# Kernel tuning notes

Measured on AMD Instinct MI355X. Metric: run time of the kernel, lower is better.

## Reference

```python
import jax, jax.numpy as jnp
import numpy as np
import math

B, N, KN, CIN, COUT, NC, DIM = 4, 8192, 16, 64, 64, 16, 3


def _linear_params(key, fan_in, fan_out):
    kw, kb = jax.random.split(key)
    bound = 1.0 / math.sqrt(fan_in)
    w = jax.random.uniform(kw, (fan_in, fan_out), jnp.float32, -bound, bound)
    b = jax.random.uniform(kb, (fan_out,), jnp.float32, -bound, bound)
    return w, b


def setup_inputs() -> dict:
    key = jax.random.key(0)
    ks = jax.random.split(key, 9)
    inp = jax.random.normal(ks[0], (B, N, CIN), jnp.float32)
    points = jax.random.uniform(ks[1], (B, N, DIM), jnp.float32)
    next_pts = jax.random.uniform(ks[2], (B, N, DIM), jnp.float32)
    indices = jax.random.randint(ks[3], (B, N, KN), 0, N, jnp.int64)
    wbound = math.sqrt(3.0) * math.sqrt(2.0 / (CIN + COUT))
    weight = jax.random.uniform(ks[4], (CIN, NC, COUT), jnp.float32, -wbound, wbound)
    bias = jnp.zeros((COUT,), jnp.float32)
    # centers: points inside the unit ball (scaled uniform cube is a faithful stand-in for a learned param init)
    centers = jax.random.uniform(ks[5], (DIM, NC), jnp.float32, -1.0, 1.0) / math.sqrt(DIM)
    l1_w, l1_b = _linear_params(ks[6], DIM * NC, 2 * NC)
    l2_w, l2_b = _linear_params(ks[7], 2 * NC, NC)
    l3_w, l3_b = _linear_params(ks[8], NC, NC)
    return {
        "inp": inp, "points": points, "next_pts": next_pts, "indices": indices,
        "weight": weight, "bias": bias, "centers": centers,
        "l1_w": l1_w, "l1_b": l1_b, "l2_w": l2_w, "l2_b": l2_b,
        "l3_w": l3_w, "l3_b": l3_b, "K": KN,
    }


def reference(inp, points, next_pts, indices, weight, bias, centers,
              l1_w, l1_b, l2_w, l2_b, l3_w, l3_b, K):
    b, n, cin = inp.shape
    bidx = jnp.arange(b)[:, None, None]
    feats = inp[bidx, indices]                                # [B, N, K, Cin] gather
    pts = points[bidx, indices] - next_pts[:, :, None, :]     # [B, N, K, D] relative coords
    # distances to kernel centers -> flatten to [B, N, K, D*NC]
    d = (pts[..., :, None] - centers).reshape(b, n, K, -1)
    d = jax.nn.relu(d @ l1_w + l1_b)
    d = jax.nn.relu(d @ l2_w + l2_b)
    d = jax.nn.relu(d @ l3_w + l3_b)                          # [B, N, K, NC]
    f = jnp.einsum('bnkc,bnkm->bncm', feats, d).reshape(b, n, -1)  # [B, N, Cin*NC]
    out = (f @ weight.reshape(-1, weight.shape[-1])) / K + bias    # [B, N, Cout]
    return out
```

## Files before the change

### kernel.cpp

```cpp
#include <hip/hip_runtime.h>

#define BB    4
#define NN    8192
#define KK    16
#define CIN   64
#define COUTC 64
#define P     16

typedef short bf16x8 __attribute__((ext_vector_type(8)));
typedef float f32x4  __attribute__((ext_vector_type(4)));
typedef float f32x2  __attribute__((ext_vector_type(2)));
typedef unsigned short u16x4 __attribute__((ext_vector_type(4)));

__device__ __forceinline__ unsigned short f2bf_rne(float f) {
    unsigned int u = __builtin_bit_cast(unsigned int, f);
    u += 0x7fffu + ((u >> 16) & 1u);
    return (unsigned short)(u >> 16);
}

__device__ __forceinline__ unsigned int pack_bf2(float lo, float hi) {
    return (unsigned int)f2bf_rne(lo) | ((unsigned int)f2bf_rne(hi) << 16);
}

__global__ __launch_bounds__(256) void prep_all(
    const float* __restrict__ inp, unsigned short* __restrict__ inp_bf,
    const float* __restrict__ W, unsigned short* __restrict__ Wt,
    const float* __restrict__ l1w, const float* __restrict__ l1b,
    const float* __restrict__ centers, float* __restrict__ A1)
{
    const int blk = blockIdx.x;
    const int t   = threadIdx.x;
    if (blk < 8192) {
        const int o  = blk * 256 + t;
        const int n  = o >> 6;
        const int q  = o & 63;
        const int r  = q >> 2;
        const int t4 = q & 3;
        inp_bf[o] = f2bf_rne(inp[n * 64 + t4 * 16 + r]);
    } else if (blk < 8448) {
        const int o    = (blk - 8192) * 256 + t;
        const int cout = o >> 10;
        const int kp   = o & 1023;
        const int m    = kp >> 6;
        const int cin  = kp & 63;
        Wt[o] = f2bf_rne(W[(cin * 16 + m) * 64 + cout] * (1.0f / 16.0f));
    } else if (t < 32) {
        float bb = l1b[t];
        float a0 = 0.f, a1 = 0.f, a2 = 0.f;
        for (int c = 0; c < 16; ++c) {
            const float w0 = l1w[(c     ) * 32 + t];
            const float w1 = l1w[(16 + c) * 32 + t];
            const float w2 = l1w[(32 + c) * 32 + t];
            a0 += w0; a1 += w1; a2 += w2;
            bb -= centers[c] * w0 + centers[16 + c] * w1 + centers[32 + c] * w2;
        }
        A1[0 * 32 + t] = a0; A1[1 * 32 + t] = a1; A1[2 * 32 + t] = a2; A1[3 * 32 + t] = bb;
    }
}

__global__ __launch_bounds__(256, 2) void ptconv_fused(
    const unsigned short* __restrict__ inp_bf,
    const float* __restrict__ points,
    const float* __restrict__ next_pts,
    const int*   __restrict__ indices,
    const unsigned short* __restrict__ Wt,
    const float* __restrict__ A1f,
    const float* __restrict__ bias,
    const float* __restrict__ l2w, const float* __restrict__ l2b,
    const float* __restrict__ l3w, const float* __restrict__ l3b,
    float* __restrict__ out)
{
    const int t    = threadIdx.x;
    const int lane = t & 63;
    const int w    = t >> 6;
    const int pt0  = blockIdx.x * P;
    const int b    = pt0 >> 13;

    __shared__ unsigned short s_u[P][512];

    const f32x2 zero2 = {0.f, 0.f};

    {
        const int p = t >> 4, k = t & 15;
        const int pt = pt0 + p;
        const int id = indices[(size_t)pt0 * KK + t];
        const float* pp = points + ((size_t)(b * NN + id)) * 3;
        const float* np = next_pts + (size_t)pt * 3;
        const float px = pp[0] - np[0];
        const float py = pp[1] - np[1];
        const float pz = pp[2] - np[2];
        const f32x2 px2 = {px, px}, py2 = {py, py}, pz2 = {pz, pz};

        const f32x2* A0  = (const f32x2*)(A1f);
        const f32x2* A1v = (const f32x2*)(A1f + 32);
        const f32x2* A2  = (const f32x2*)(A1f + 64);
        const f32x2* A3  = (const f32x2*)(A1f + 96);
        f32x2 h1[16];
        #pragma unroll
        for (int j = 0; j < 16; ++j) {
            f32x2 a = __builtin_elementwise_fma(pz2, A2[j], A3[j]);
            a = __builtin_elementwise_fma(py2, A1v[j], a);
            a = __builtin_elementwise_fma(px2, A0[j], a);
            h1[j] = __builtin_elementwise_max(a, zero2);
        }

        f32x2 h2[8];
        {
            const f32x2* b2p = (const f32x2*)l2b;
            #pragma unroll
            for (int j = 0; j < 8; ++j) h2[j] = b2p[j];
        }
        #pragma unroll
        for (int i = 0; i < 32; ++i) {
            const float hv = h1[i >> 1][i & 1];
            const f32x2 hvv = {hv, hv};
            const f32x2* wr = (const f32x2*)(l2w + i * 16);
            #pragma unroll
            for (int j = 0; j < 8; ++j)
                h2[j] = __builtin_elementwise_fma(hvv, wr[j], h2[j]);
        }
        #pragma unroll
        for (int j = 0; j < 8; ++j) h2[j] = __builtin_elementwise_max(h2[j], zero2);

        f32x2 h3v[8];
        {
            const f32x2* b3p = (const f32x2*)l3b;
            #pragma unroll
            for (int j = 0; j < 8; ++j) h3v[j] = b3p[j];
        }
        #pragma unroll
        for (int i = 0; i < 16; ++i) {
            const float hv = h2[i >> 1][i & 1];
            const f32x2 hvv = {hv, hv};
            const f32x2* wr = (const f32x2*)(l3w + i * 16);
            #pragma unroll
            for (int j = 0; j < 8; ++j)
                h3v[j] = __builtin_elementwise_fma(hvv, wr[j], h3v[j]);
        }
        char* ub = (char*)s_u;
        const unsigned int hsw = ((unsigned)(p & 3)) << 5;
        #pragma unroll
        for (int j = 0; j < 8; ++j) {
            const f32x2 v = __builtin_elementwise_max(h3v[j], zero2);
            const unsigned int b0 = ((unsigned)(p * 1024 + (2 * j    ) * 32 + k * 2)) ^ hsw;
            const unsigned int b1 = ((unsigned)(p * 1024 + (2 * j + 1) * 32 + k * 2)) ^ hsw;
            *(unsigned short*)(ub + b0) = f2bf_rne(v[0]);
            *(unsigned short*)(ub + b1) = f2bf_rne(v[1]);
        }
    }
    __threadfence_block();

    uint2 holdA[2][2], holdB[2][2];
    {
        const int arow = lane & 15;
        const int hi   = lane >> 4;
        const int kg   = (hi & 1) * 8;
        const unsigned short* ibase = inp_bf + (size_t)b * NN * 64;
        const int* idxg = indices + (size_t)pt0 * KK;
        const bf16x8 vzero = {0, 0, 0, 0, 0, 0, 0, 0};
        char* fbb = (char*)s_u;

        #pragma unroll
        for (int pr = 0; pr < 2; ++pr) {
            const int pA  = w * 4 + pr * 2;
            const int pB  = pA + 1;
            const int myp = (hi < 2) ? pA : pB;

            const int4 i0 = *(const int4*)&idxg[myp * 16 + kg];
            const int4 i1 = *(const int4*)&idxg[myp * 16 + kg + 4];
            const int ids[8] = {i0.x, i0.y, i0.z, i0.w, i1.x, i1.y, i1.z, i1.w};

            u16x4 rows[8];
            #pragma unroll
            for (int jj = 0; jj < 8; ++jj)
                rows[jj] = *(const u16x4*)(ibase + (size_t)ids[jj] * 64 + arow * 4);

            const unsigned int hb = ((unsigned)(myp * 1024 + arow * 32 + kg * 2))
                                    ^ (((unsigned)(myp & 3)) << 5);
            const bf16x8 vfull = *(const bf16x8*)((const char*)s_u + hb);
            const bf16x8 bfA = (hi < 2) ? vfull : vzero;
            const bf16x8 bfB = (hi < 2) ? vzero : vfull;

            #pragma unroll
            for (int tile = 0; tile < 4; ++tile) {
                bf16x8 af;
                #pragma unroll
                for (int jj = 0; jj < 8; ++jj) af[jj] = (short)rows[jj][tile];
                const f32x4 z4 = {0.f, 0.f, 0.f, 0.f};
                const f32x4 dA = __builtin_amdgcn_mfma_f32_16x16x32_bf16(af, bfA, z4, 0, 0, 0);
                const f32x4 dB = __builtin_amdgcn_mfma_f32_16x16x32_bf16(af, bfB, z4, 0, 0, 0);
                const uint2 vA = make_uint2(pack_bf2(dA[0], dA[1]), pack_bf2(dA[2], dA[3]));
                const uint2 vB = make_uint2(pack_bf2(dB[0], dB[1]), pack_bf2(dB[2], dB[3]));
                if (tile < 2) {
                    const unsigned int baseo = (unsigned)(arow * 64 + tile * 32 + hi * 8);
                    const unsigned int offA = ((unsigned)(pA * 1024) + baseo)
                                              ^ (((unsigned)((pA & 7) ^ (arow & 7))) << 4);
                    const unsigned int offB = ((unsigned)(pB * 1024) + baseo)
                                              ^ (((unsigned)((pB & 7) ^ (arow & 7))) << 4);
                    *(uint2*)(fbb + offA) = vA;
                    *(uint2*)(fbb + offB) = vB;
                } else {
                    holdA[pr][tile - 2] = vA;
                    holdB[pr][tile - 2] = vB;
                }
            }
        }
    }
    __syncthreads();

    {
        const int arow = lane & 15;
        const int hi   = lane >> 4;
        const unsigned short* wb = Wt + (size_t)(w * 16 + arow) * 1024 + hi * 8;
        const char* fbb = (const char*)s_u;
        f32x4 acc = {0.f, 0.f, 0.f, 0.f};

        #pragma unroll
        for (int m = 0; m < 16; ++m) {
            const unsigned int xr = ((unsigned)((arow & 7) ^ (m & 7))) << 4;
            const bf16x8 av = *(const bf16x8*)(fbb +
                (((unsigned)(arow * 1024 + m * 64 + hi * 16)) ^ xr));
            const bf16x8 bv = *(const bf16x8*)(wb + m * 64);
            acc = __builtin_amdgcn_mfma_f32_16x16x32_bf16(av, bv, acc, 0, 0, 0);
        }
        __syncthreads();

        {
            char* fbw = (char*)s_u;
            #pragma unroll
            for (int pr = 0; pr < 2; ++pr) {
                const int pA = w * 4 + pr * 2;
                const int pB = pA + 1;
                #pragma unroll
                for (int t2 = 0; t2 < 2; ++t2) {
                    const unsigned int baseo = (unsigned)(arow * 64 + t2 * 32 + hi * 8);
                    const unsigned int offA = ((unsigned)(pA * 1024) + baseo)
                                              ^ (((unsigned)((pA & 7) ^ (arow & 7))) << 4);
                    const unsigned int offB = ((unsigned)(pB * 1024) + baseo)
                                              ^ (((unsigned)((pB & 7) ^ (arow & 7))) << 4);
                    *(uint2*)(fbw + offA) = holdA[pr][t2];
                    *(uint2*)(fbw + offB) = holdB[pr][t2];
                }
            }
        }
        __syncthreads();

        #pragma unroll
        for (int m = 0; m < 16; ++m) {
            const unsigned int xr = ((unsigned)((arow & 7) ^ (m & 7))) << 4;
            const bf16x8 av = *(const bf16x8*)(fbb +
                (((unsigned)(arow * 1024 + m * 64 + hi * 16)) ^ xr));
            const bf16x8 bv = *(const bf16x8*)(wb + m * 64 + 32);
            acc = __builtin_amdgcn_mfma_f32_16x16x32_bf16(av, bv, acc, 0, 0, 0);
        }

        const float bvs = bias[w * 16 + arow];
        #pragma unroll
        for (int r = 0; r < 4; ++r) {
            const int prow = hi * 4 + r;
            out[((size_t)(pt0 + prow)) * 64 + w * 16 + arow] = acc[r] + bvs;
        }
    }
}

extern "C" void kernel_launch(void* const* d_in, const int* in_sizes, int n_in,
                              void* d_out, int out_size, void* d_ws, size_t ws_size,
                              hipStream_t stream) {
    const float* inp      = (const float*)d_in[0];
    const float* points   = (const float*)d_in[1];
    const float* next_pts = (const float*)d_in[2];
    const int*   indices  = (const int*)  d_in[3];
    const float* weight   = (const float*)d_in[4];
    const float* bias     = (const float*)d_in[5];
    const float* centers  = (const float*)d_in[6];
    const float* l1w      = (const float*)d_in[7];
    const float* l1b      = (const float*)d_in[8];
    const float* l2w      = (const float*)d_in[9];
    const float* l2b      = (const float*)d_in[10];
    const float* l3w      = (const float*)d_in[11];
    const float* l3b      = (const float*)d_in[12];
    float* outp = (float*)d_out;

    unsigned short* Wt    = (unsigned short*)d_ws;
    float*          A1f   = (float*)((char*)d_ws + 131072);
    unsigned short* inpbf = (unsigned short*)((char*)d_ws + (1 << 20));

    prep_all<<<8449, 256, 0, stream>>>(inp, inpbf, weight, Wt,
                                       l1w, l1b, centers, A1f);

    const int grid = (BB * NN) / P;
    ptconv_fused<<<grid, 256, 0, stream>>>(inpbf, points, next_pts, indices,
                                           Wt, A1f, bias,
                                           l2w, l2b, l3w, l3b, outp);
}
```

Measured before the change: 57.03 us.

## Process 32 points per block, reusing weight fragments across two MFMA tiles

Doubles the points handled per block from 16 to 32. Each thread now runs the per-neighbour MLP for two neighbours, each wave gathers and transposes twice as many point pairs, and the final GEMM issues two MFMAs per loaded weight fragment. This halves the global weight reads per point and the per-block overhead. In exchange it doubles shared memory and the held registers per block and halves the grid size, which may reduce occupancy.

Result: faster. 54.51 us (-4.4%).

```diff
diff --git a/kernel.cpp b/kernel.cpp
--- a/kernel.cpp
+++ b/kernel.cpp
@@ -5,7 +5,7 @@
 #define KK    16
 #define CIN   64
 #define COUTC 64
-#define P     16
+#define P     32
 
 typedef short bf16x8 __attribute__((ext_vector_type(8)));
 typedef float f32x4  __attribute__((ext_vector_type(4)));
@@ -81,76 +81,84 @@
     const f32x2 zero2 = {0.f, 0.f};
 
     {
-        const int p = t >> 4, k = t & 15;
+        const int p  = w * 8 + (lane >> 3);
+        const int kb = lane & 7;
         const int pt = pt0 + p;
-        const int id = indices[(size_t)pt0 * KK + t];
-        const float* pp = points + ((size_t)(b * NN + id)) * 3;
         const float* np = next_pts + (size_t)pt * 3;
-        const float px = pp[0] - np[0];
-        const float py = pp[1] - np[1];
-        const float pz = pp[2] - np[2];
-        const f32x2 px2 = {px, px}, py2 = {py, py}, pz2 = {pz, pz};
+        const float nx = np[0], ny = np[1], nz = np[2];
 
         const f32x2* A0  = (const f32x2*)(A1f);
         const f32x2* A1v = (const f32x2*)(A1f + 32);
         const f32x2* A2  = (const f32x2*)(A1f + 64);
         const f32x2* A3  = (const f32x2*)(A1f + 96);
-        f32x2 h1[16];
-        #pragma unroll
-        for (int j = 0; j < 16; ++j) {
-            f32x2 a = __builtin_elementwise_fma(pz2, A2[j], A3[j]);
-            a = __builtin_elementwise_fma(py2, A1v[j], a);
-            a = __builtin_elementwise_fma(px2, A0[j], a);
-            h1[j] = __builtin_elementwise_max(a, zero2);
-        }
-
-        f32x2 h2[8];
-        {
-            const f32x2* b2p = (const f32x2*)l2b;
-            #pragma unroll
-            for (int j = 0; j < 8; ++j) h2[j] = b2p[j];
-        }
-        #pragma unroll
-        for (int i = 0; i < 32; ++i) {
-            const float hv = h1[i >> 1][i & 1];
-            const f32x2 hvv = {hv, hv};
-            const f32x2* wr = (const f32x2*)(l2w + i * 16);
-            #pragma unroll
-            for (int j = 0; j < 8; ++j)
-                h2[j] = __builtin_elementwise_fma(hvv, wr[j], h2[j]);
-        }
-        #pragma unroll
-        for (int j = 0; j < 8; ++j) h2[j] = __builtin_elementwise_max(h2[j], zero2);
-
-        f32x2 h3v[8];
-        {
-            const f32x2* b3p = (const f32x2*)l3b;
-            #pragma unroll
-            for (int j = 0; j < 8; ++j) h3v[j] = b3p[j];
-        }
-        #pragma unroll
-        for (int i = 0; i < 16; ++i) {
-            const float hv = h2[i >> 1][i & 1];
-            const f32x2 hvv = {hv, hv};
-            const f32x2* wr = (const f32x2*)(l3w + i * 16);
-            #pragma unroll
-            for (int j = 0; j < 8; ++j)
-                h3v[j] = __builtin_elementwise_fma(hvv, wr[j], h3v[j]);
-        }
-        char* ub = (char*)s_u;
-        const unsigned int hsw = ((unsigned)(p & 3)) << 5;
-        #pragma unroll
-        for (int j = 0; j < 8; ++j) {
-            const f32x2 v = __builtin_elementwise_max(h3v[j], zero2);
-            const unsigned int b0 = ((unsigned)(p * 1024 + (2 * j    ) * 32 + k * 2)) ^ hsw;
-            const unsigned int b1 = ((unsigned)(p * 1024 + (2 * j + 1) * 32 + k * 2)) ^ hsw;
-            *(unsigned short*)(ub + b0) = f2bf_rne(v[0]);
-            *(unsigned short*)(ub + b1) = f2bf_rne(v[1]);
+
+        #pragma unroll
+        for (int ii = 0; ii < 2; ++ii) {
+            const int k  = kb + ii * 8;
+            const int id = indices[(size_t)pt0 * KK + p * 16 + k];
+            const float* pp = points + ((size_t)(b * NN + id)) * 3;
+            const float px = pp[0] - nx;
+            const float py = pp[1] - ny;
+            const float pz = pp[2] - nz;
+            const f32x2 px2 = {px, px}, py2 = {py, py}, pz2 = {pz, pz};
+
+            f32x2 h1[16];
+            #pragma unroll
+            for (int j = 0; j < 16; ++j) {
+                f32x2 a = __builtin_elementwise_fma(pz2, A2[j], A3[j]);
+                a = __builtin_elementwise_fma(py2, A1v[j], a);
+                a = __builtin_elementwise_fma(px2, A0[j], a);
+                h1[j] = __builtin_elementwise_max(a, zero2);
+            }
+
+            f32x2 h2[8];
+            {
+                const f32x2* b2p = (const f32x2*)l2b;
+                #pragma unroll
+                for (int j = 0; j < 8; ++j) h2[j] = b2p[j];
+            }
+            #pragma unroll
+            for (int i = 0; i < 32; ++i) {
+                const float hv = h1[i >> 1][i & 1];
+                const f32x2 hvv = {hv, hv};
+                const f32x2* wr = (const f32x2*)(l2w + i * 16);
+                #pragma unroll
+                for (int j = 0; j < 8; ++j)
+                    h2[j] = __builtin_elementwise_fma(hvv, wr[j], h2[j]);
+            }
+            #pragma unroll
+            for (int j = 0; j < 8; ++j) h2[j] = __builtin_elementwise_max(h2[j], zero2);
+
+            f32x2 h3v[8];
+            {
+                const f32x2* b3p = (const f32x2*)l3b;
+                #pragma unroll
+                for (int j = 0; j < 8; ++j) h3v[j] = b3p[j];
+            }
+            #pragma unroll
+            for (int i = 0; i < 16; ++i) {
+                const float hv = h2[i >> 1][i & 1];
+                const f32x2 hvv = {hv, hv};
+                const f32x2* wr = (const f32x2*)(l3w + i * 16);
+                #pragma unroll
+                for (int j = 0; j < 8; ++j)
+                    h3v[j] = __builtin_elementwise_fma(hvv, wr[j], h3v[j]);
+            }
+            char* ub = (char*)s_u;
+            const unsigned int hsw = ((unsigned)(p & 3)) << 5;
+            #pragma unroll
+            for (int j = 0; j < 8; ++j) {
+                const f32x2 v = __builtin_elementwise_max(h3v[j], zero2);
+                const unsigned int b0 = ((unsigned)(p * 1024 + (2 * j    ) * 32 + k * 2)) ^ hsw;
+                const unsigned int b1 = ((unsigned)(p * 1024 + (2 * j + 1) * 32 + k * 2)) ^ hsw;
+                *(unsigned short*)(ub + b0) = f2bf_rne(v[0]);
+                *(unsigned short*)(ub + b1) = f2bf_rne(v[1]);
+            }
         }
     }
     __threadfence_block();
 
-    uint2 holdA[2][2], holdB[2][2];
+    uint2 holdA[4][2], holdB[4][2];
     {
         const int arow = lane & 15;
         const int hi   = lane >> 4;
@@ -161,8 +169,8 @@
         char* fbb = (char*)s_u;
 
         #pragma unroll
-        for (int pr = 0; pr < 2; ++pr) {
-            const int pA  = w * 4 + pr * 2;
+        for (int pr = 0; pr < 4; ++pr) {
+            const int pA  = w * 8 + pr * 2;
             const int pB  = pA + 1;
             const int myp = (hi < 2) ? pA : pB;
 
@@ -213,23 +221,27 @@
         const int hi   = lane >> 4;
         const unsigned short* wb = Wt + (size_t)(w * 16 + arow) * 1024 + hi * 8;
         const char* fbb = (const char*)s_u;
-        f32x4 acc = {0.f, 0.f, 0.f, 0.f};
+        f32x4 acc0 = {0.f, 0.f, 0.f, 0.f};
+        f32x4 acc1 = {0.f, 0.f, 0.f, 0.f};
 
         #pragma unroll
         for (int m = 0; m < 16; ++m) {
             const unsigned int xr = ((unsigned)((arow & 7) ^ (m & 7))) << 4;
-            const bf16x8 av = *(const bf16x8*)(fbb +
+            const bf16x8 bv  = *(const bf16x8*)(wb + m * 64);
+            const bf16x8 av0 = *(const bf16x8*)(fbb +
                 (((unsigned)(arow * 1024 + m * 64 + hi * 16)) ^ xr));
-            const bf16x8 bv = *(const bf16x8*)(wb + m * 64);
-            acc = __builtin_amdgcn_mfma_f32_16x16x32_bf16(av, bv, acc, 0, 0, 0);
+            const bf16x8 av1 = *(const bf16x8*)(fbb +
+                (((unsigned)((16 + arow) * 1024 + m * 64 + hi * 16)) ^ xr));
+            acc0 = __builtin_amdgcn_mfma_f32_16x16x32_bf16(av0, bv, acc0, 0, 0, 0);
+            acc1 = __builtin_amdgcn_mfma_f32_16x16x32_bf16(av1, bv, acc1, 0, 0, 0);
         }
         __syncthreads();
 
         {
             char* fbw = (char*)s_u;
             #pragma unroll
-            for (int pr = 0; pr < 2; ++pr) {
-                const int pA = w * 4 + pr * 2;
+            for (int pr = 0; pr < 4; ++pr) {
+                const int pA = w * 8 + pr * 2;
                 const int pB = pA + 1;
                 #pragma unroll
                 for (int t2 = 0; t2 < 2; ++t2) {
@@ -248,17 +260,21 @@
         #pragma unroll
         for (int m = 0; m < 16; ++m) {
             const unsigned int xr = ((unsigned)((arow & 7) ^ (m & 7))) << 4;
-            const bf16x8 av = *(const bf16x8*)(fbb +
+            const bf16x8 bv  = *(const bf16x8*)(wb + m * 64 + 32);
+            const bf16x8 av0 = *(const bf16x8*)(fbb +
                 (((unsigned)(arow * 1024 + m * 64 + hi * 16)) ^ xr));
-            const bf16x8 bv = *(const bf16x8*)(wb + m * 64 + 32);
-            acc = __builtin_amdgcn_mfma_f32_16x16x32_bf16(av, bv, acc, 0, 0, 0);
+            const bf16x8 av1 = *(const bf16x8*)(fbb +
+                (((unsigned)((16 + arow) * 1024 + m * 64 + hi * 16)) ^ xr));
+            acc0 = __builtin_amdgcn_mfma_f32_16x16x32_bf16(av0, bv, acc0, 0, 0, 0);
+            acc1 = __builtin_amdgcn_mfma_f32_16x16x32_bf16(av1, bv, acc1, 0, 0, 0);
         }
 
         const float bvs = bias[w * 16 + arow];
         #pragma unroll
         for (int r = 0; r < 4; ++r) {
             const int prow = hi * 4 + r;
-            out[((size_t)(pt0 + prow)) * 64 + w * 16 + arow] = acc[r] + bvs;
+            out[((size_t)(pt0 + prow)) * 64 + w * 16 + arow]      = acc0[r] + bvs;
+            out[((size_t)(pt0 + 16 + prow)) * 64 + w * 16 + arow] = acc1[r] + bvs;
         }
     }
 }
```

## Run the per-neighbor MLP layers 2 and 3 on bf16 MFMA via LDS staging

Applied to the files above, without the earlier changes.

The second and third layers of the per-neighbor weight MLP were scalar fp32 FMA loops per thread (about 768 FMAs each). They now run as bf16 16x16x32 MFMAs. Layer-1 activations are packed to bf16 and staged in a per-wave LDS region, and pre-transposed bf16 copies of l2w/l3w (zero-padded for layer 3) are built in the prep kernel. This removes a large scalar ALU and register cost in exchange for extra LDS round trips, wave-local fences, and bf16 rounding of the intermediate activations.

After: 53.13 us. 1.07x faster.

```diff
diff --git a/kernel.cpp b/kernel.cpp
--- a/kernel.cpp
+++ b/kernel.cpp
@@ -26,7 +26,9 @@
     const float* __restrict__ inp, unsigned short* __restrict__ inp_bf,
     const float* __restrict__ W, unsigned short* __restrict__ Wt,
     const float* __restrict__ l1w, const float* __restrict__ l1b,
-    const float* __restrict__ centers, float* __restrict__ A1)
+    const float* __restrict__ centers, float* __restrict__ A1,
+    const float* __restrict__ l2w, const float* __restrict__ l3w,
+    unsigned short* __restrict__ Wt2, unsigned short* __restrict__ Wt3)
 {
     const int blk = blockIdx.x;
     const int t   = threadIdx.x;
@@ -44,17 +46,32 @@
         const int m    = kp >> 6;
         const int cin  = kp & 63;
         Wt[o] = f2bf_rne(W[(cin * 16 + m) * 64 + cout] * (1.0f / 16.0f));
-    } else if (t < 32) {
-        float bb = l1b[t];
-        float a0 = 0.f, a1 = 0.f, a2 = 0.f;
-        for (int c = 0; c < 16; ++c) {
-            const float w0 = l1w[(c     ) * 32 + t];
-            const float w1 = l1w[(16 + c) * 32 + t];
-            const float w2 = l1w[(32 + c) * 32 + t];
-            a0 += w0; a1 += w1; a2 += w2;
-            bb -= centers[c] * w0 + centers[16 + c] * w1 + centers[32 + c] * w2;
-        }
-        A1[0 * 32 + t] = a0; A1[1 * 32 + t] = a1; A1[2 * 32 + t] = a2; A1[3 * 32 + t] = bb;
+    } else if (blk == 8448) {
+        if (t < 32) {
+            float bb = l1b[t];
+            float a0 = 0.f, a1 = 0.f, a2 = 0.f;
+            for (int c = 0; c < 16; ++c) {
+                const float w0 = l1w[(c     ) * 32 + t];
+                const float w1 = l1w[(16 + c) * 32 + t];
+                const float w2 = l1w[(32 + c) * 32 + t];
+                a0 += w0; a1 += w1; a2 += w2;
+                bb -= centers[c] * w0 + centers[16 + c] * w1 + centers[32 + c] * w2;
+            }
+            A1[0 * 32 + t] = a0; A1[1 * 32 + t] = a1; A1[2 * 32 + t] = a2; A1[3 * 32 + t] = bb;
+        }
+    } else {
+        for (int i = t; i < 1024; i += 256) {
+            if (i < 512) {
+                const int l = i >> 3, j = i & 7;
+                const int k = (l >> 4) * 8 + j, col = l & 15;
+                Wt2[i] = f2bf_rne(l2w[k * 16 + col]);
+            } else {
+                const int i3 = i - 512;
+                const int l = i3 >> 3, j = i3 & 7;
+                const int k = (l >> 4) * 8 + j, col = l & 15;
+                Wt3[i3] = (k < 16) ? f2bf_rne(l3w[k * 16 + col]) : (unsigned short)0;
+            }
+        }
     }
 }
 
@@ -64,10 +81,11 @@
     const float* __restrict__ next_pts,
     const int*   __restrict__ indices,
     const unsigned short* __restrict__ Wt,
+    const unsigned short* __restrict__ Wt2,
+    const unsigned short* __restrict__ Wt3,
     const float* __restrict__ A1f,
     const float* __restrict__ bias,
-    const float* __restrict__ l2w, const float* __restrict__ l2b,
-    const float* __restrict__ l3w, const float* __restrict__ l3b,
+    const float* __restrict__ l2b, const float* __restrict__ l3b,
     float* __restrict__ out)
 {
     const int t    = threadIdx.x;
@@ -78,10 +96,14 @@
 
     __shared__ unsigned short s_u[P][512];
 
+    char* const wb = (char*)s_u + w * 4096;
     const f32x2 zero2 = {0.f, 0.f};
-
-    {
-        const int p = t >> 4, k = t & 15;
+    const f32x4 z4 = {0.f, 0.f, 0.f, 0.f};
+    const int arow = lane & 15;
+    const int hi   = lane >> 4;
+
+    {
+        const int p = t >> 4;
         const int pt = pt0 + p;
         const int id = indices[(size_t)pt0 * KK + t];
         const float* pp = points + ((size_t)(b * NN + id)) * 3;
@@ -95,65 +117,86 @@
         const f32x2* A1v = (const f32x2*)(A1f + 32);
         const f32x2* A2  = (const f32x2*)(A1f + 64);
         const f32x2* A3  = (const f32x2*)(A1f + 96);
-        f32x2 h1[16];
+        unsigned int pk[16];
         #pragma unroll
         for (int j = 0; j < 16; ++j) {
             f32x2 a = __builtin_elementwise_fma(pz2, A2[j], A3[j]);
             a = __builtin_elementwise_fma(py2, A1v[j], a);
             a = __builtin_elementwise_fma(px2, A0[j], a);
-            h1[j] = __builtin_elementwise_max(a, zero2);
-        }
-
-        f32x2 h2[8];
-        {
-            const f32x2* b2p = (const f32x2*)l2b;
-            #pragma unroll
-            for (int j = 0; j < 8; ++j) h2[j] = b2p[j];
-        }
-        #pragma unroll
-        for (int i = 0; i < 32; ++i) {
-            const float hv = h1[i >> 1][i & 1];
-            const f32x2 hvv = {hv, hv};
-            const f32x2* wr = (const f32x2*)(l2w + i * 16);
-            #pragma unroll
-            for (int j = 0; j < 8; ++j)
-                h2[j] = __builtin_elementwise_fma(hvv, wr[j], h2[j]);
-        }
-        #pragma unroll
-        for (int j = 0; j < 8; ++j) h2[j] = __builtin_elementwise_max(h2[j], zero2);
-
-        f32x2 h3v[8];
-        {
-            const f32x2* b3p = (const f32x2*)l3b;
-            #pragma unroll
-            for (int j = 0; j < 8; ++j) h3v[j] = b3p[j];
-        }
-        #pragma unroll
-        for (int i = 0; i < 16; ++i) {
-            const float hv = h2[i >> 1][i & 1];
-            const f32x2 hvv = {hv, hv};
-            const f32x2* wr = (const f32x2*)(l3w + i * 16);
-            #pragma unroll
-            for (int j = 0; j < 8; ++j)
-                h3v[j] = __builtin_elementwise_fma(hvv, wr[j], h3v[j]);
-        }
-        char* ub = (char*)s_u;
-        const unsigned int hsw = ((unsigned)(p & 3)) << 5;
-        #pragma unroll
-        for (int j = 0; j < 8; ++j) {
-            const f32x2 v = __builtin_elementwise_max(h3v[j], zero2);
-            const unsigned int b0 = ((unsigned)(p * 1024 + (2 * j    ) * 32 + k * 2)) ^ hsw;
-            const unsigned int b1 = ((unsigned)(p * 1024 + (2 * j + 1) * 32 + k * 2)) ^ hsw;
-            *(unsigned short*)(ub + b0) = f2bf_rne(v[0]);
-            *(unsigned short*)(ub + b1) = f2bf_rne(v[1]);
+            a = __builtin_elementwise_max(a, zero2);
+            pk[j] = pack_bf2(a[0], a[1]);
+        }
+        #pragma unroll
+        for (int c = 0; c < 4; ++c) {
+            const unsigned int off = (unsigned)(lane * 64)
+                + ((((unsigned)c) * 16u) ^ (((unsigned)(lane & 3)) << 4));
+            *(uint4*)(wb + off) = make_uint4(pk[4*c], pk[4*c+1], pk[4*c+2], pk[4*c+3]);
         }
     }
     __threadfence_block();
 
+    {
+        const bf16x8 b2 = *(const bf16x8*)(Wt2 + lane * 8);
+        const float bias2 = l2b[arow];
+        uint2 h2sv[4];
+        #pragma unroll
+        for (int T = 0; T < 4; ++T) {
+            const int row = T * 16 + arow;
+            const unsigned int off = (unsigned)(row * 64)
+                + ((((unsigned)hi) * 16u) ^ (((unsigned)(row & 3)) << 4));
+            const bf16x8 a = *(const bf16x8*)(wb + off);
+            const f32x4 d = __builtin_amdgcn_mfma_f32_16x16x32_bf16(a, b2, z4, 0, 0, 0);
+            h2sv[T].x = pack_bf2(fmaxf(d[0] + bias2, 0.f), fmaxf(d[1] + bias2, 0.f));
+            h2sv[T].y = pack_bf2(fmaxf(d[2] + bias2, 0.f), fmaxf(d[3] + bias2, 0.f));
+        }
+        __threadfence_block();
+        #pragma unroll
+        for (int T = 0; T < 4; ++T) {
+            const unsigned short v0 = (unsigned short)(h2sv[T].x & 0xffffu);
+            const unsigned short v1 = (unsigned short)(h2sv[T].x >> 16);
+            const unsigned short v2 = (unsigned short)(h2sv[T].y & 0xffffu);
+            const unsigned short v3 = (unsigned short)(h2sv[T].y >> 16);
+            const int R0 = T * 16 + hi * 4;
+            *(unsigned short*)(wb + ((unsigned)((R0+0) * 32 + arow * 2) ^ (((unsigned)((R0+0) & 1)) << 4))) = v0;
+            *(unsigned short*)(wb + ((unsigned)((R0+1) * 32 + arow * 2) ^ (((unsigned)((R0+1) & 1)) << 4))) = v1;
+            *(unsigned short*)(wb + ((unsigned)((R0+2) * 32 + arow * 2) ^ (((unsigned)((R0+2) & 1)) << 4))) = v2;
+            *(unsigned short*)(wb + ((unsigned)((R0+3) * 32 + arow * 2) ^ (((unsigned)((R0+3) & 1)) << 4))) = v3;
+        }
+    }
+    __threadfence_block();
+
+    {
+        const bf16x8 b3 = *(const bf16x8*)(Wt3 + lane * 8);
+        const float bias3 = l3b[arow];
+        uint2 hsave[4];
+        #pragma unroll
+        for (int T = 0; T < 4; ++T) {
+            const int row = T * 16 + arow;
+            const unsigned int off = ((unsigned)(row * 32 + hi * 16)) ^ (((unsigned)(row & 1)) << 4);
+            const bf16x8 a = *(const bf16x8*)(wb + off);
+            const f32x4 d = __builtin_amdgcn_mfma_f32_16x16x32_bf16(a, b3, z4, 0, 0, 0);
+            hsave[T].x = pack_bf2(fmaxf(d[0] + bias3, 0.f), fmaxf(d[1] + bias3, 0.f));
+            hsave[T].y = pack_bf2(fmaxf(d[2] + bias3, 0.f), fmaxf(d[3] + bias3, 0.f));
+        }
+        __threadfence_block();
+        #pragma unroll
+        for (int T = 0; T < 4; ++T) {
+            const unsigned int xw = ((unsigned)(T & 3)) << 5;
+            const unsigned short h0  = (unsigned short)(hsave[T].x & 0xffffu);
+            const unsigned short h1v = (unsigned short)(hsave[T].x >> 16);
+            const unsigned short h2v = (unsigned short)(hsave[T].y & 0xffffu);
+            const unsigned short h3v = (unsigned short)(hsave[T].y >> 16);
+            const unsigned int base = (unsigned)(T * 1024 + arow * 32 + hi * 8);
+            *(unsigned short*)(wb + ((base + 0) ^ xw)) = h0;
+            *(unsigned short*)(wb + ((base + 2) ^ xw)) = h1v;
+            *(unsigned short*)(wb + ((base + 4) ^ xw)) = h2v;
+            *(unsigned short*)(wb + ((base + 6) ^ xw)) = h3v;
+        }
+    }
+    __threadfence_block();
+
     uint2 holdA[2][2], holdB[2][2];
     {
-        const int arow = lane & 15;
-        const int hi   = lane >> 4;
         const int kg   = (hi & 1) * 8;
         const unsigned short* ibase = inp_bf + (size_t)b * NN * 64;
         const int* idxg = indices + (size_t)pt0 * KK;
@@ -186,7 +229,6 @@
                 bf16x8 af;
                 #pragma unroll
                 for (int jj = 0; jj < 8; ++jj) af[jj] = (short)rows[jj][tile];
-                const f32x4 z4 = {0.f, 0.f, 0.f, 0.f};
                 const f32x4 dA = __builtin_amdgcn_mfma_f32_16x16x32_bf16(af, bfA, z4, 0, 0, 0);
                 const f32x4 dB = __builtin_amdgcn_mfma_f32_16x16x32_bf16(af, bfB, z4, 0, 0, 0);
                 const uint2 vA = make_uint2(pack_bf2(dA[0], dA[1]), pack_bf2(dA[2], dA[3]));
@@ -209,9 +251,7 @@
     __syncthreads();
 
     {
-        const int arow = lane & 15;
-        const int hi   = lane >> 4;
-        const unsigned short* wb = Wt + (size_t)(w * 16 + arow) * 1024 + hi * 8;
+        const unsigned short* wtb = Wt + (size_t)(w * 16 + arow) * 1024 + hi * 8;
         const char* fbb = (const char*)s_u;
         f32x4 acc = {0.f, 0.f, 0.f, 0.f};
 
@@ -220,7 +260,7 @@
             const unsigned int xr = ((unsigned)((arow & 7) ^ (m & 7))) << 4;
             const bf16x8 av = *(const bf16x8*)(fbb +
                 (((unsigned)(arow * 1024 + m * 64 + hi * 16)) ^ xr));
-            const bf16x8 bv = *(const bf16x8*)(wb + m * 64);
+            const bf16x8 bv = *(const bf16x8*)(wtb + m * 64);
             acc = __builtin_amdgcn_mfma_f32_16x16x32_bf16(av, bv, acc, 0, 0, 0);
         }
         __syncthreads();
@@ -250,7 +290,7 @@
             const unsigned int xr = ((unsigned)((arow & 7) ^ (m & 7))) << 4;
             const bf16x8 av = *(const bf16x8*)(fbb +
                 (((unsigned)(arow * 1024 + m * 64 + hi * 16)) ^ xr));
-            const bf16x8 bv = *(const bf16x8*)(wb + m * 64 + 32);
+            const bf16x8 bv = *(const bf16x8*)(wtb + m * 64 + 32);
             acc = __builtin_amdgcn_mfma_f32_16x16x32_bf16(av, bv, acc, 0, 0, 0);
         }
 
@@ -283,13 +323,16 @@
 
     unsigned short* Wt    = (unsigned short*)d_ws;
     float*          A1f   = (float*)((char*)d_ws + 131072);
+    unsigned short* Wt2   = (unsigned short*)((char*)d_ws + 132096);
+    unsigned short* Wt3   = (unsigned short*)((char*)d_ws + 133120);
     unsigned short* inpbf = (unsigned short*)((char*)d_ws + (1 << 20));
 
-    prep_all<<<8449, 256, 0, stream>>>(inp, inpbf, weight, Wt,
-                                       l1w, l1b, centers, A1f);
+    prep_all<<<8450, 256, 0, stream>>>(inp, inpbf, weight, Wt,
+                                       l1w, l1b, centers, A1f,
+                                       l2w, l3w, Wt2, Wt3);
 
     const int grid = (BB * NN) / P;
     ptconv_fused<<<grid, 256, 0, stream>>>(inpbf, points, next_pts, indices,
-                                           Wt, A1f, bias,
-                                           l2w, l2b, l3w, l3b, outp);
-}
+                                           Wt, Wt2, Wt3, A1f, bias,
+                                           l2b, l3b, outp);
+}
```
